# Kernel tuning notes

Measured on AMD Instinct MI355X. Metric: run time of the kernel, lower is better.

The kernel has to match this reference:

```python
import jax, jax.numpy as jnp
import numpy as np

N_E = 4096      # n_embed
E_DIM = 64      # embed_dim
BETA = 0.25
DECAY = 0.99
EPS = 1e-05


def setup_inputs() -> dict:
    key = jax.random.key(0)
    k1, k2, k3, k4 = jax.random.split(key, 4)
    z = jax.random.normal(k1, (4, 64, 16, 32, 32), dtype=jnp.float32)
    # codebook initialized uniform(-1/n_e, 1/n_e) as in the torch module
    embed_w = jax.random.uniform(k2, (N_E, E_DIM), dtype=jnp.float32,
                                 minval=-1.0 / N_E, maxval=1.0 / N_E)
    cluster_size = jax.random.uniform(k3, (N_E,), dtype=jnp.float32)
    embed_avg = jax.random.normal(k4, (N_E, E_DIM), dtype=jnp.float32) * 0.01
    return {"z": z, "embed_w": embed_w, "cluster_size": cluster_size,
            "embed_avg": embed_avg}


def reference(z, embed_w, cluster_size, embed_avg):
    sg = jax.lax.stop_gradient
    # b c d h w -> b d h w c
    zp = jnp.transpose(z, (0, 2, 3, 4, 1))
    zf = zp.reshape(-1, E_DIM)                      # [N, e_dim]
    n_tok = zf.shape[0]
    # squared L2 distances to every code: [N, n_e]
    d = ((zf * zf).sum(axis=1, keepdims=True)
         + (embed_w * embed_w).sum(axis=1)
         - 2.0 * jnp.einsum('bd,nd->bn', zf, embed_w))
    idx = jnp.argmin(d, axis=1)                     # [N]
    z_q = embed_w[idx].reshape(zp.shape)            # codebook gather
    # perplexity from code-usage histogram (== mean of one-hot encodings)
    counts = jnp.zeros((N_E,), zf.dtype).at[idx].add(1.0)
    avg_probs = counts / n_tok
    perplexity = jnp.exp(-jnp.sum(avg_probs * jnp.log(avg_probs + 1e-10)))
    # EMA buffer updates (training mode; pure buffer math, no gradient flow)
    embed_sum = jnp.zeros((N_E, E_DIM), zf.dtype).at[idx].add(sg(zf))  # one_hot.T @ zf
    new_cs = cluster_size * DECAY + (1.0 - DECAY) * counts
    new_ea = embed_avg * DECAY + (1.0 - DECAY) * embed_sum
    n = new_cs.sum()
    smoothed_cs = (new_cs + EPS) / (n + N_E * EPS) * n
    new_embed = new_ea / smoothed_cs[:, None]
    # commitment loss and straight-through estimator
    loss = BETA * jnp.mean((sg(z_q) - zp) ** 2)
    z_q_st = zp + sg(z_q - zp)
    out = jnp.transpose(z_q_st, (0, 4, 1, 2, 3))    # b d h w c -> b c d h w
    return (out, loss, perplexity, idx, new_embed, new_cs, new_ea)
```

## Files before the change

### kernel.cpp

```cpp
#include <hip/hip_runtime.h>

static constexpr int NE   = 4096;
static constexpr int ED   = 64;
static constexpr int NTOK = 65536;
static constexpr int NCHUNK = 16;
static constexpr int CPC  = NE / NCHUNK;

typedef float f32x2 __attribute__((ext_vector_type(2)));

static __device__ __forceinline__ f32x2 pkfma(f32x2 a, f32x2 b, f32x2 c) {
#if __has_builtin(__builtin_elementwise_fma)
    return __builtin_elementwise_fma(a, b, c);
#else
    f32x2 r;
    r.x = fmaf(a.x, b.x, c.x);
    r.y = fmaf(a.y, b.y, c.y);
    return r;
#endif
}

static constexpr long O_OUT  = 0;
static constexpr long O_LOSS = 4194304;
static constexpr long O_PERP = 4194305;
static constexpr long O_IDX  = 4194306;
static constexpr long O_NEMB = 4259842;
static constexpr long O_NCS  = 4521986;
static constexpr long O_NEA  = 4526082;

static constexpr size_t W_ACC   = 0;
static constexpr size_t W_CNT   = 32;
static constexpr size_t W_CUR   = 16416;
static constexpr size_t W_OFF   = 32800;
static constexpr size_t W_BSQ   = 49184;
static constexpr size_t W_IDX   = 65568;
static constexpr size_t W_BKT   = 327712;
static constexpr size_t W_LOSSP = 589856;
static constexpr size_t W_PKD   = 720928;
static constexpr size_t W_ZERO_BYTES = 32800;
static constexpr size_t W_PKD_BYTES  = 524288;

__global__ __launch_bounds__(256) void kBsq(const float* __restrict__ e,
                                            float* __restrict__ bsq) {
    int n = blockIdx.x * 256 + threadIdx.x;
    const float* er = e + (n << 6);
    float a0 = 0.f, a1 = 0.f, a2 = 0.f, a3 = 0.f;
#pragma unroll
    for (int k = 0; k < ED; k += 4) {
        a0 = fmaf(er[k+0], er[k+0], a0);
        a1 = fmaf(er[k+1], er[k+1], a1);
        a2 = fmaf(er[k+2], er[k+2], a2);
        a3 = fmaf(er[k+3], er[k+3], a3);
    }
    bsq[n] = (a0 + a1) + (a2 + a3);
}

#define Z_EACH(F) \
    F(0)  F(1)  F(2)  F(3)  F(4)  F(5)  F(6)  F(7)  \
    F(8)  F(9)  F(10) F(11) F(12) F(13) F(14) F(15) \
    F(16) F(17) F(18) F(19) F(20) F(21) F(22) F(23) \
    F(24) F(25) F(26) F(27) F(28) F(29) F(30) F(31)

__global__ __launch_bounds__(256, 4) void kArgmin(const float* __restrict__ z,
                                                  const float* __restrict__ e,
                                                  const float* __restrict__ bsq,
                                                  unsigned long long* __restrict__ packed) {
    int bid = blockIdx.x;
    int tb = bid >> 4;
    int chunk = bid & 15;
    int t = tb * 256 + threadIdx.x;
    int b = t >> 14;
    int s = t & 16383;
    const float* zp = z + (long)b * 1048576 + s;

#define Z_LOAD(J) f32x2 Z##J; Z##J.x = zp[(2*J)   * 16384]; \
                              Z##J.y = zp[(2*J+1) * 16384];
    Z_EACH(Z_LOAD)
#undef Z_LOAD

    f32x2 aa0 = {0.f, 0.f}, aa1 = {0.f, 0.f};
#define Z_ASUM(J) { if ((J & 1) == 0) aa0 = pkfma(Z##J, Z##J, aa0); \
                    else              aa1 = pkfma(Z##J, Z##J, aa1); }
    Z_EACH(Z_ASUM)
#undef Z_ASUM
    float A = (aa0.x + aa0.y) + (aa1.x + aa1.y);

    float best = __builtin_inff();
    int bidx = 0;
    int c0 = chunk * CPC;
    for (int n = c0; n < c0 + CPC; ++n) {
        int nu = __builtin_amdgcn_readfirstlane(n);
        const f32x2* __restrict__ er2 = (const f32x2*)(e + (nu << 6));
        float bq = bsq[nu];
        f32x2 c0v = {0.f, 0.f}, c1v = {0.f, 0.f};
#define Z_DOT(J) { if ((J & 1) == 0) c0v = pkfma(Z##J, er2[J], c0v); \
                   else              c1v = pkfma(Z##J, er2[J], c1v); }
        Z_EACH(Z_DOT)
#undef Z_DOT
        float dot = (c0v.x + c0v.y) + (c1v.x + c1v.y);
        float d = fmaf(-2.0f, dot, A + bq);
        if (d < best) { best = d; bidx = n; }
    }
    unsigned long long pk =
        ((unsigned long long)__float_as_uint(best) << 32) | (unsigned)bidx;
    atomicMin(&packed[t], pk);
}

__global__ __launch_bounds__(256) void kFinish(const unsigned long long* __restrict__ packed,
                                               float* __restrict__ outIdxF,
                                               int* __restrict__ wsIdx,
                                               unsigned* __restrict__ counts) {
    int t = blockIdx.x * 256 + threadIdx.x;
    int idx = (int)(unsigned)(packed[t] & 0xFFFFFFFFull);
    outIdxF[t] = (float)idx;
    wsIdx[t]   = idx;
    atomicAdd(&counts[idx], 1u);
}

__global__ __launch_bounds__(256) void kOffsets(const unsigned* __restrict__ counts,
                                                unsigned* __restrict__ offsets) {
    __shared__ unsigned psum[256];
    int tid = threadIdx.x;
    unsigned local[16];
    unsigned s = 0;
#pragma unroll
    for (int j = 0; j < 16; ++j) { local[j] = s; s += counts[tid * 16 + j]; }
    psum[tid] = s;
    __syncthreads();
    unsigned base = 0;
    for (int i = 0; i < tid; ++i) base += psum[i];
#pragma unroll
    for (int j = 0; j < 16; ++j) offsets[tid * 16 + j] = base + local[j];
}

__global__ __launch_bounds__(256) void kScatter(const int* __restrict__ wsIdx,
                                                const unsigned* __restrict__ offsets,
                                                unsigned* __restrict__ cursor,
                                                int* __restrict__ bucket) {
    int t = blockIdx.x * 256 + threadIdx.x;
    int idx = wsIdx[t];
    unsigned pos = atomicAdd(&cursor[idx], 1u);
    bucket[offsets[idx] + pos] = t;
}

__global__ __launch_bounds__(256) void kEpilogue(const float* __restrict__ z,
                                                 const float* __restrict__ e,
                                                 const int* __restrict__ wsIdx,
                                                 float* __restrict__ out,
                                                 double* __restrict__ lossPart) {
    __shared__ double lp[4];
    long g = (long)blockIdx.x * 256 + threadIdx.x;
    int b = (int)(g >> 20);
    int r = (int)(g & 1048575);
    int k = r >> 14;
    int s = r & 16383;
    int t = (b << 14) | s;

    float zv = z[g];
    int n = wsIdx[t];
    float eq = e[(n << 6) + k];
    float diff = eq - zv;
    out[g] = zv + diff;

    double sq = (double)diff * (double)diff;
#pragma unroll
    for (int o = 32; o > 0; o >>= 1) sq += __shfl_down(sq, o);
    if ((threadIdx.x & 63) == 0) lp[threadIdx.x >> 6] = sq;
    __syncthreads();
    if (threadIdx.x == 0) lossPart[blockIdx.x] = (lp[0] + lp[1]) + (lp[2] + lp[3]);
}

__global__ __launch_bounds__(256) void kLoss(const double* __restrict__ lossPart,
                                             double* __restrict__ acc) {
    __shared__ double lp[4];
    double s = 0.0;
    for (int j = 0; j < 64; ++j) s += lossPart[threadIdx.x + j * 256];
#pragma unroll
    for (int o = 32; o > 0; o >>= 1) s += __shfl_down(s, o);
    if ((threadIdx.x & 63) == 0) lp[threadIdx.x >> 6] = s;
    __syncthreads();
    if (threadIdx.x == 0) acc[0] = (lp[0] + lp[1]) + (lp[2] + lp[3]);
}

__global__ __launch_bounds__(256) void kEma1(const float* __restrict__ cs,
                                             const unsigned* __restrict__ counts,
                                             float* __restrict__ outNcs,
                                             double* __restrict__ acc) {
    int n = blockIdx.x * 256 + threadIdx.x;
    float cf = (float)counts[n];
    float p1 = cs[n] * 0.99f;
    float p2 = 0.01f * cf;
    float ncs = p1 + p2;
    outNcs[n] = ncs;
    float p = cf * (1.0f / 65536.0f);
    float term = p * logf(p + 1e-10f);
    double dn = (double)ncs, dt = (double)term;
#pragma unroll
    for (int o = 32; o > 0; o >>= 1) { dn += __shfl_down(dn, o); dt += __shfl_down(dt, o); }
    if ((threadIdx.x & 63) == 0) {
        atomicAdd(&acc[1], dn);
        atomicAdd(&acc[2], dt);
    }
}

__global__ __launch_bounds__(64) void kEsumEma2(const float* __restrict__ z,
                                                const float* __restrict__ ea,
                                                const int* __restrict__ bucket,
                                                const unsigned* __restrict__ offsets,
                                                const unsigned* __restrict__ counts,
                                                const float* __restrict__ ncsArr,
                                                const double* __restrict__ acc,
                                                float* __restrict__ outNemb,
                                                float* __restrict__ outNea,
                                                float* __restrict__ outLoss,
                                                float* __restrict__ outPerp) {
    int n = blockIdx.x;
    int k = threadIdx.x;
    unsigned off = offsets[n];
    unsigned cnt = counts[n];
    float es = 0.f;
    for (unsigned i = 0; i < cnt; ++i) {
        int t = bucket[off + i];
        int b = t >> 14;
        int s = t & 16383;
        es += z[(long)b * 1048576 + k * 16384 + s];
    }
    float nea = ea[(n << 6) + k] * 0.99f + 0.01f * es;
    outNea[(n << 6) + k] = nea;
    float nt = (float)acc[1];
    float ncs = ncsArr[n];
    float sc = ((ncs + 1e-5f) / (nt + 0.04096f)) * nt;
    outNemb[(n << 6) + k] = nea / sc;
    if (n == 0 && k == 0) {
        double m = acc[0] / 4194304.0;
        outLoss[0] = 0.25f * (float)m;
        outPerp[0] = (float)exp(-acc[2]);
    }
}

extern "C" void kernel_launch(void* const* d_in, const int* in_sizes, int n_in,
                              void* d_out, int out_size, void* d_ws, size_t ws_size,
                              hipStream_t stream) {
    const float* z  = (const float*)d_in[0];
    const float* ew = (const float*)d_in[1];
    const float* cs = (const float*)d_in[2];
    const float* ea = (const float*)d_in[3];
    float* out = (float*)d_out;
    char* ws = (char*)d_ws;

    double*   acc    = (double*)(ws + W_ACC);
    unsigned* counts = (unsigned*)(ws + W_CNT);
    unsigned* cursor = (unsigned*)(ws + W_CUR);
    unsigned* offs   = (unsigned*)(ws + W_OFF);
    float*    bsq    = (float*)(ws + W_BSQ);
    int*      wsIdx  = (int*)(ws + W_IDX);
    int*      bucket = (int*)(ws + W_BKT);
    double*   lossP  = (double*)(ws + W_LOSSP);
    unsigned long long* packed = (unsigned long long*)(ws + W_PKD);

    hipMemsetAsync(ws, 0, W_ZERO_BYTES, stream);
    hipMemsetAsync(ws + W_PKD, 0xFF, W_PKD_BYTES, stream);
    kBsq<<<NE / 256, 256, 0, stream>>>(ew, bsq);
    kArgmin<<<(NTOK / 256) * NCHUNK, 256, 0, stream>>>(z, ew, bsq, packed);
    kFinish<<<NTOK / 256, 256, 0, stream>>>(packed, out + O_IDX, wsIdx, counts);
    kOffsets<<<1, 256, 0, stream>>>(counts, offs);
    kScatter<<<NTOK / 256, 256, 0, stream>>>(wsIdx, offs, cursor, bucket);
    kEpilogue<<<16384, 256, 0, stream>>>(z, ew, wsIdx, out + O_OUT, lossP);
    kLoss<<<1, 256, 0, stream>>>(lossP, acc);
    kEma1<<<NE / 256, 256, 0, stream>>>(cs, counts, out + O_NCS, acc);
    kEsumEma2<<<NE, 64, 0, stream>>>(z, ea, bucket, offs, counts, out + O_NCS, acc,
                                     out + O_NEMB, out + O_NEA,
                                     out + O_LOSS, out + O_PERP);
}
```

Baseline: 509.3 us.

## Pack codebook rows with norms and hand-write scalar-load argmin inner loop

Builds an augmented codebook with each 64-float row followed by its squared norm in a 68-float stride. The argmin inner loop is rewritten in inline assembly so the row and norm arrive through a few wide scalar loads and feed packed FMAs directly. This removes the separate norm load and compiler scheduling overhead from the hot loop. The tradeoff is a single lgkmcnt wait per code with no prefetching, so scalar memory latency is exposed on every iteration, and the hardcoded SGPR/VGPR clobbers are fragile against register allocation.

```diff
diff --git a/kernel.cpp b/kernel.cpp
--- a/kernel.cpp
+++ b/kernel.cpp
@@ -6,7 +6,8 @@
 static constexpr int NCHUNK = 16;
 static constexpr int CPC  = NE / NCHUNK;
 
-typedef float f32x2 __attribute__((ext_vector_type(2)));
+typedef float  f32x2 __attribute__((ext_vector_type(2)));
+typedef float  f32x4 __attribute__((ext_vector_type(4)));
 
 static __device__ __forceinline__ f32x2 pkfma(f32x2 a, f32x2 b, f32x2 c) {
 #if __has_builtin(__builtin_elementwise_fma)
@@ -31,18 +32,19 @@
 static constexpr size_t W_CNT   = 32;
 static constexpr size_t W_CUR   = 16416;
 static constexpr size_t W_OFF   = 32800;
-static constexpr size_t W_BSQ   = 49184;
-static constexpr size_t W_IDX   = 65568;
-static constexpr size_t W_BKT   = 327712;
-static constexpr size_t W_LOSSP = 589856;
-static constexpr size_t W_PKD   = 720928;
+static constexpr size_t W_IDX   = 49184;
+static constexpr size_t W_BKT   = 311328;
+static constexpr size_t W_LOSSP = 573472;
+static constexpr size_t W_PKD   = 704544;
+static constexpr size_t W_AUG   = 1228832;
 static constexpr size_t W_ZERO_BYTES = 32800;
 static constexpr size_t W_PKD_BYTES  = 524288;
 
-__global__ __launch_bounds__(256) void kBsq(const float* __restrict__ e,
-                                            float* __restrict__ bsq) {
+__global__ __launch_bounds__(256) void kAug(const float* __restrict__ e,
+                                            float* __restrict__ aug) {
     int n = blockIdx.x * 256 + threadIdx.x;
     const float* er = e + (n << 6);
+    float* row = aug + (long)n * 68;
     float a0 = 0.f, a1 = 0.f, a2 = 0.f, a3 = 0.f;
 #pragma unroll
     for (int k = 0; k < ED; k += 4) {
@@ -51,7 +53,10 @@
         a2 = fmaf(er[k+2], er[k+2], a2);
         a3 = fmaf(er[k+3], er[k+3], a3);
     }
-    bsq[n] = (a0 + a1) + (a2 + a3);
+#pragma unroll
+    for (int k = 0; k < 16; ++k)
+        ((f32x4*)row)[k] = ((const f32x4*)er)[k];
+    row[64] = (a0 + a1) + (a2 + a3);
 }
 
 #define Z_EACH(F) \
@@ -60,9 +65,19 @@
     F(16) F(17) F(18) F(19) F(20) F(21) F(22) F(23) \
     F(24) F(25) F(26) F(27) F(28) F(29) F(30) F(31)
 
+#define SCLOBBERS \
+    "s32","s33","s34","s35","s36","s37","s38","s39", \
+    "s40","s41","s42","s43","s44","s45","s46","s47", \
+    "s48","s49","s50","s51","s52","s53","s54","s55", \
+    "s56","s57","s58","s59","s60","s61","s62","s63", \
+    "s64","s65","s66","s67","s68","s69","s70","s71", \
+    "s72","s73","s74","s75","s76","s77","s78","s79", \
+    "s80","s81","s82","s83","s84","s85","s86","s87", \
+    "s88","s89","s90","s91","s92","s93","s94","s95", \
+    "s96","s97","s98","s99","s100"
+
 __global__ __launch_bounds__(256, 4) void kArgmin(const float* __restrict__ z,
-                                                  const float* __restrict__ e,
-                                                  const float* __restrict__ bsq,
+                                                  const float* __restrict__ aug,
                                                   unsigned long long* __restrict__ packed) {
     int bid = blockIdx.x;
     int tb = bid >> 4;
@@ -84,22 +99,84 @@
 #undef Z_ASUM
     float A = (aa0.x + aa0.y) + (aa1.x + aa1.y);
 
+    int c0i = chunk * CPC;
+    int cend = c0i + CPC;
+    const float* rowPtr = aug + (long)c0i * 68;
+
     float best = __builtin_inff();
-    int bidx = 0;
-    int c0 = chunk * CPC;
-    for (int n = c0; n < c0 + CPC; ++n) {
-        int nu = __builtin_amdgcn_readfirstlane(n);
-        const f32x2* __restrict__ er2 = (const f32x2*)(e + (nu << 6));
-        float bq = bsq[nu];
-        f32x2 c0v = {0.f, 0.f}, c1v = {0.f, 0.f};
-#define Z_DOT(J) { if ((J & 1) == 0) c0v = pkfma(Z##J, er2[J], c0v); \
-                   else              c1v = pkfma(Z##J, er2[J], c1v); }
-        Z_EACH(Z_DOT)
-#undef Z_DOT
-        float dot = (c0v.x + c0v.y) + (c1v.x + c1v.y);
-        float d = fmaf(-2.0f, dot, A + bq);
-        if (d < best) { best = d; bidx = n; }
-    }
+    int bidx = c0i;
+
+    asm volatile(
+        "s_mov_b64 s[98:99], %[ptr]\n\t"
+        "s_mov_b32 s97, %[n0]\n\t"
+        "s_mov_b32 s100, %[ne]\n\t"
+        "1:\n\t"
+        "s_load_dwordx16 s[32:47], s[98:99], 0x0\n\t"
+        "s_load_dwordx16 s[48:63], s[98:99], 0x40\n\t"
+        "s_load_dwordx16 s[64:79], s[98:99], 0x80\n\t"
+        "s_load_dwordx16 s[80:95], s[98:99], 0xc0\n\t"
+        "s_load_dword s96, s[98:99], 0x100\n\t"
+        "s_waitcnt lgkmcnt(0)\n\t"
+        "v_pk_mul_f32 v[48:49], %[z0], s[32:33]\n\t"
+        "v_pk_mul_f32 v[50:51], %[z1], s[34:35]\n\t"
+        "v_pk_fma_f32 v[48:49], %[z2], s[36:37], v[48:49]\n\t"
+        "v_pk_fma_f32 v[50:51], %[z3], s[38:39], v[50:51]\n\t"
+        "v_pk_fma_f32 v[48:49], %[z4], s[40:41], v[48:49]\n\t"
+        "v_pk_fma_f32 v[50:51], %[z5], s[42:43], v[50:51]\n\t"
+        "v_pk_fma_f32 v[48:49], %[z6], s[44:45], v[48:49]\n\t"
+        "v_pk_fma_f32 v[50:51], %[z7], s[46:47], v[50:51]\n\t"
+        "v_pk_fma_f32 v[48:49], %[z8], s[48:49], v[48:49]\n\t"
+        "v_pk_fma_f32 v[50:51], %[z9], s[50:51], v[50:51]\n\t"
+        "v_pk_fma_f32 v[48:49], %[z10], s[52:53], v[48:49]\n\t"
+        "v_pk_fma_f32 v[50:51], %[z11], s[54:55], v[50:51]\n\t"
+        "v_pk_fma_f32 v[48:49], %[z12], s[56:57], v[48:49]\n\t"
+        "v_pk_fma_f32 v[50:51], %[z13], s[58:59], v[50:51]\n\t"
+        "v_pk_fma_f32 v[48:49], %[z14], s[60:61], v[48:49]\n\t"
+        "v_pk_fma_f32 v[50:51], %[z15], s[62:63], v[50:51]\n\t"
+        "v_pk_fma_f32 v[48:49], %[z16], s[64:65], v[48:49]\n\t"
+        "v_pk_fma_f32 v[50:51], %[z17], s[66:67], v[50:51]\n\t"
+        "v_pk_fma_f32 v[48:49], %[z18], s[68:69], v[48:49]\n\t"
+        "v_pk_fma_f32 v[50:51], %[z19], s[70:71], v[50:51]\n\t"
+        "v_pk_fma_f32 v[48:49], %[z20], s[72:73], v[48:49]\n\t"
+        "v_pk_fma_f32 v[50:51], %[z21], s[74:75], v[50:51]\n\t"
+        "v_pk_fma_f32 v[48:49], %[z22], s[76:77], v[48:49]\n\t"
+        "v_pk_fma_f32 v[50:51], %[z23], s[78:79], v[50:51]\n\t"
+        "v_pk_fma_f32 v[48:49], %[z24], s[80:81], v[48:49]\n\t"
+        "v_pk_fma_f32 v[50:51], %[z25], s[82:83], v[50:51]\n\t"
+        "v_pk_fma_f32 v[48:49], %[z26], s[84:85], v[48:49]\n\t"
+        "v_pk_fma_f32 v[50:51], %[z27], s[86:87], v[50:51]\n\t"
+        "v_pk_fma_f32 v[48:49], %[z28], s[88:89], v[48:49]\n\t"
+        "v_pk_fma_f32 v[50:51], %[z29], s[90:91], v[50:51]\n\t"
+        "v_pk_fma_f32 v[48:49], %[z30], s[92:93], v[48:49]\n\t"
+        "v_pk_fma_f32 v[50:51], %[z31], s[94:95], v[50:51]\n\t"
+        "v_add_f32 v52, v48, v49\n\t"
+        "v_add_f32 v53, v50, v51\n\t"
+        "v_add_f32 v52, v52, v53\n\t"
+        "v_add_f32 v53, s96, %[A]\n\t"
+        "v_fma_f32 v54, -2.0, v52, v53\n\t"
+        "v_mov_b32 v55, s97\n\t"
+        "v_cmp_lt_f32 vcc, v54, %[best]\n\t"
+        "v_cndmask_b32 %[best], %[best], v54, vcc\n\t"
+        "v_cndmask_b32 %[bidx], %[bidx], v55, vcc\n\t"
+        "s_add_u32 s98, s98, 272\n\t"
+        "s_addc_u32 s99, s99, 0\n\t"
+        "s_add_u32 s97, s97, 1\n\t"
+        "s_cmp_lt_u32 s97, s100\n\t"
+        "s_cbranch_scc1 1b\n\t"
+        : [best]"+v"(best), [bidx]"+v"(bidx)
+        : [z0]"v"(Z0),  [z1]"v"(Z1),  [z2]"v"(Z2),  [z3]"v"(Z3),
+          [z4]"v"(Z4),  [z5]"v"(Z5),  [z6]"v"(Z6),  [z7]"v"(Z7),
+          [z8]"v"(Z8),  [z9]"v"(Z9),  [z10]"v"(Z10), [z11]"v"(Z11),
+          [z12]"v"(Z12), [z13]"v"(Z13), [z14]"v"(Z14), [z15]"v"(Z15),
+          [z16]"v"(Z16), [z17]"v"(Z17), [z18]"v"(Z18), [z19]"v"(Z19),
+          [z20]"v"(Z20), [z21]"v"(Z21), [z22]"v"(Z22), [z23]"v"(Z23),
+          [z24]"v"(Z24), [z25]"v"(Z25), [z26]"v"(Z26), [z27]"v"(Z27),
+          [z28]"v"(Z28), [z29]"v"(Z29), [z30]"v"(Z30), [z31]"v"(Z31),
+          [A]"v"(A), [ptr]"s"(rowPtr), [n0]"s"(c0i), [ne]"s"(cend)
+        : SCLOBBERS,
+          "v48","v49","v50","v51","v52","v53","v54","v55",
+          "vcc","scc","memory");
+
     unsigned long long pk =
         ((unsigned long long)__float_as_uint(best) << 32) | (unsigned)bidx;
     atomicMin(&packed[t], pk);
@@ -251,16 +328,16 @@
     unsigned* counts = (unsigned*)(ws + W_CNT);
     unsigned* cursor = (unsigned*)(ws + W_CUR);
     unsigned* offs   = (unsigned*)(ws + W_OFF);
-    float*    bsq    = (float*)(ws + W_BSQ);
     int*      wsIdx  = (int*)(ws + W_IDX);
     int*      bucket = (int*)(ws + W_BKT);
     double*   lossP  = (double*)(ws + W_LOSSP);
     unsigned long long* packed = (unsigned long long*)(ws + W_PKD);
+    float*    aug    = (float*)(ws + W_AUG);
 
     hipMemsetAsync(ws, 0, W_ZERO_BYTES, stream);
     hipMemsetAsync(ws + W_PKD, 0xFF, W_PKD_BYTES, stream);
-    kBsq<<<NE / 256, 256, 0, stream>>>(ew, bsq);
-    kArgmin<<<(NTOK / 256) * NCHUNK, 256, 0, stream>>>(z, ew, bsq, packed);
+    kAug<<<NE / 256, 256, 0, stream>>>(ew, aug);
+    kArgmin<<<(NTOK / 256) * NCHUNK, 256, 0, stream>>>(z, aug, packed);
     kFinish<<<NTOK / 256, 256, 0, stream>>>(packed, out + O_IDX, wsIdx, counts);
     kOffsets<<<1, 256, 0, stream>>>(counts, offs);
     kScatter<<<NTOK / 256, 256, 0, stream>>>(wsIdx, offs, cursor, bucket);
```

Measured after the change: 511.0 us. About the same (+0.3%).
